# Optimization experiments

Hardware: AMD Instinct MI355X
Metric: run time of the kernel (lower is better)

The kernel has to match this reference:

```python
import jax, jax.numpy as jnp
import numpy as np
from jax import lax

B, T, I, H, O = 1000, 100, 264, 100, 264


def _lstm_cell(x, h, c, Wih, Whh, bih, bhh):
    # PyTorch gate order: i, f, g, o
    gates = x @ Wih.T + bih + h @ Whh.T + bhh  # [B, 4H]
    i, f, g, o = jnp.split(gates, 4, axis=-1)
    i = jax.nn.sigmoid(i)
    f = jax.nn.sigmoid(f)
    g = jnp.tanh(g)
    o = jax.nn.sigmoid(o)
    c = f * c + i * g
    h = o * jnp.tanh(c)
    return h, c


def _encode(src, Wih, Whh, bih, bhh):
    # src: [B, T, I] -> final (h, c), each [B, H]
    x_t = jnp.swapaxes(src, 0, 1)  # [T, B, I]
    h0 = jnp.zeros((src.shape[0], H), src.dtype)
    c0 = jnp.zeros((src.shape[0], H), src.dtype)

    def step(carry, x):
        h, c = carry
        h, c = _lstm_cell(x, h, c, Wih, Whh, bih, bhh)
        return (h, c), None

    (h, c), _ = lax.scan(step, (h0, c0), x_t)
    return h, c


def _decode(h, c, Wih, Whh, bih, bhh, fcW, fcb, batch, steps):
    x0 = jnp.zeros((batch, I), h.dtype)

    def step(carry, _):
        x, hh, cc = carry
        hh, cc = _lstm_cell(x, hh, cc, Wih, Whh, bih, bhh)
        pred = hh @ fcW.T + fcb  # [B, O]
        return (pred, hh, cc), pred

    _, preds = lax.scan(step, (x0, h, c), None, length=steps)
    return jnp.swapaxes(preds, 0, 1)  # [B, T, O]


def setup_inputs():
    key = jax.random.key(0)
    ks = jax.random.split(key, 20)
    bound = 1.0 / np.sqrt(H)

    def u(k, shp):
        return jax.random.uniform(k, shp, jnp.float32, -bound, bound)

    inp = {
        "src": jax.random.normal(ks[0], (B, T, I), jnp.float32),
        "trg": jax.random.normal(ks[1], (B, T, I), jnp.float32),
        "enc_Wih": u(ks[2], (4 * H, I)), "enc_Whh": u(ks[3], (4 * H, H)),
        "enc_bih": u(ks[4], (4 * H,)), "enc_bhh": u(ks[5], (4 * H,)),
        "pd_Wih": u(ks[6], (4 * H, I)), "pd_Whh": u(ks[7], (4 * H, H)),
        "pd_bih": u(ks[8], (4 * H,)), "pd_bhh": u(ks[9], (4 * H,)),
        "pd_fcW": u(ks[10], (O, H)), "pd_fcb": u(ks[11], (O,)),
        "rd_Wih": u(ks[12], (4 * H, I)), "rd_Whh": u(ks[13], (4 * H, H)),
        "rd_bih": u(ks[14], (4 * H,)), "rd_bhh": u(ks[15], (4 * H,)),
        "rd_fcW": u(ks[16], (O, H)), "rd_fcb": u(ks[17], (O,)),
    }
    return inp


def reference(src, trg, enc_Wih, enc_Whh, enc_bih, enc_bhh,
              pd_Wih, pd_Whh, pd_bih, pd_bhh, pd_fcW, pd_fcb,
              rd_Wih, rd_Whh, rd_bih, rd_bhh, rd_fcW, rd_fcb):
    batch, steps, _ = src.shape
    h, c = _encode(src, enc_Wih, enc_Whh, enc_bih, enc_bhh)

    predict_output = _decode(h, c, pd_Wih, pd_Whh, pd_bih, pd_bhh,
                             pd_fcW, pd_fcb, batch, steps)
    predict_loss = jnp.mean((predict_output - trg) ** 2)

    reconstruct_output = _decode(h, c, rd_Wih, rd_Whh, rd_bih, rd_bhh,
                                 rd_fcW, rd_fcb, batch, steps)
    src_rev = src[:, ::-1, :]
    reconstruct_loss = jnp.mean((reconstruct_output - src_rev) ** 2)

    return reconstruct_loss, predict_loss
```

## Files before the change

### kernel.cpp

```cpp
#include <hip/hip_runtime.h>
#include <math.h>

#define NB 1000
#define NT 100
#define NI 264
#define NH 100
#define NO 264
#define NG 400
#define KE 364
#define DM 4
#define NDB 250
#define EDM 4
#define DTH 192
#define XM 16

__device__ __forceinline__ float sigm(float x){ return 1.f / (1.f + __expf(-x)); }
__device__ __forceinline__ float tanh_fast(float x){
    float e = __expf(-2.f * x);
    return 2.f / (1.f + e) - 1.f;
}

#define FMA4(acc, hv, wv) acc += hv.x*wv.x + hv.y*wv.y + hv.z*wv.z + hv.w*wv.w;

#define W_LIST(OP) OP(0) OP(1) OP(2) OP(3) OP(4) OP(5) OP(6) OP(7) OP(8) OP(9) \
                   OP(10) OP(11) OP(12) OP(13) OP(14) OP(15) OP(16) OP(17) OP(18) OP(19) \
                   OP(20) OP(21) OP(22) OP(23) OP(24)

#define DECL_W(i)    float4 w##i = make_float4(0.f, 0.f, 0.f, 0.f);
#define LOADW_ENC(i) w##i = WhhT4[(i) * NG + n];

#define ROW4K(wv, kk) { float4 hq; \
    hq = ((const float4*)sh_h[0])[kk]; FMA4(a0, hq, wv) \
    hq = ((const float4*)sh_h[1])[kk]; FMA4(a1, hq, wv) \
    hq = ((const float4*)sh_h[2])[kk]; FMA4(a2, hq, wv) \
    hq = ((const float4*)sh_h[3])[kk]; FMA4(a3, hq, wv) }

#define ESTEP(i) ROW4K(w##i, i)


__global__ void prep_T4(const float* __restrict__ in, float* __restrict__ out, int N, int K)
{
    int idx = blockIdx.x * 256 + threadIdx.x;
    if (idx >= N * K) return;
    int j  = idx & 3;
    int n  = (idx >> 2) % N;
    int k  = (idx / (4 * N)) * 4 + j;
    out[idx] = in[n * K + k];
}

__global__ void prep_encT(const float* __restrict__ Wih, const float* __restrict__ Whh,
                          float* __restrict__ out)
{
    int idx = blockIdx.x * 256 + threadIdx.x;
    if (idx >= NG * KE) return;
    int j  = idx & 3;
    int n  = (idx >> 2) % NG;
    int k  = (idx / (4 * NG)) * 4 + j;
    out[idx] = (k < NI) ? Wih[n * NI + k] : Whh[n * NH + (k - NI)];
}

__global__ void prep_wdec(const float* __restrict__ Wih, const float* __restrict__ Whh,
                          const float* __restrict__ fcW, float* __restrict__ WdecT)
{
    int idx = blockIdx.x * 256 + threadIdx.x;
    if (idx >= NG * NH) return;
    int n = idx / NH, k = idx - n * NH;
    float acc = Whh[idx];
    const float* wr = Wih + (size_t)n * NI;
    for (int o = 0; o < NI; ++o) acc = fmaf(wr[o], fcW[o * NH + k], acc);
    WdecT[((k >> 2) * NG + n) * 4 + (k & 3)] = acc;
}

__global__ void prep_bias(const float* __restrict__ pb1, const float* __restrict__ pb2,
                          const float* __restrict__ pW,  const float* __restrict__ pfb,
                          const float* __restrict__ rb1, const float* __restrict__ rb2,
                          const float* __restrict__ rW,  const float* __restrict__ rfb,
                          const float* __restrict__ eb1, const float* __restrict__ eb2,
                          float* __restrict__ b0_p, float* __restrict__ bdec_p,
                          float* __restrict__ b0_r, float* __restrict__ bdec_r,
                          float* __restrict__ bcat, float* __restrict__ loss)
{
    int tid = blockIdx.x * 256 + threadIdx.x;
    if (tid < 2) loss[tid] = 0.f;
    if (tid < NG) bcat[tid] = eb1[tid] + eb2[tid];
    if (tid >= 2 * NG) return;
    int dd = tid / NG, n = tid - dd * NG;
    const float* b1 = dd ? rb1 : pb1;
    const float* b2 = dd ? rb2 : pb2;
    const float* W  = dd ? rW  : pW;
    const float* fb = dd ? rfb : pfb;
    float base = b1[n] + b2[n];
    float acc = base;
    const float* wr = W + (size_t)n * NI;
    for (int o = 0; o < NI; ++o) acc = fmaf(wr[o], fb[o], acc);
    if (dd){ b0_r[n] = base; bdec_r[n] = acc; }
    else   { b0_p[n] = base; bdec_p[n] = acc; }
}


__global__ __launch_bounds__(512) void xp_kernel(const float* __restrict__ src,
                                                 const float4* __restrict__ WihT4,
                                                 float* __restrict__ xp)
{
    __shared__ float sh_x[XM * NI];
    __shared__ float sh_o[XM * NG];
    const int tid = threadIdx.x;
    const size_t bt0 = (size_t)blockIdx.x * XM;
    for (int i = tid; i < XM * NI; i += 512) sh_x[i] = src[bt0 * NI + i];
    __syncthreads();
    const bool act = tid < NG;
    const int n = act ? tid : 0;
    float a0=0,a1=0,a2=0,a3=0,a4=0,a5=0,a6=0,a7=0,
          a8=0,a9=0,a10=0,a11=0,a12=0,a13=0,a14=0,a15=0;
    if (act){
        #pragma unroll 3
        for (int k4 = 0; k4 < NI / 4; ++k4){
            float4 wq = WihT4[k4 * NG + n];
            float4 hq;
            #define XROW(r, acc) hq = ((const float4*)(sh_x + (r) * NI))[k4]; FMA4(acc, hq, wq)
            XROW(0,a0)  XROW(1,a1)  XROW(2,a2)  XROW(3,a3)
            XROW(4,a4)  XROW(5,a5)  XROW(6,a6)  XROW(7,a7)
            XROW(8,a8)  XROW(9,a9)  XROW(10,a10) XROW(11,a11)
            XROW(12,a12) XROW(13,a13) XROW(14,a14) XROW(15,a15)
            #undef XROW
        }
        sh_o[0*NG+n]=a0;   sh_o[1*NG+n]=a1;   sh_o[2*NG+n]=a2;   sh_o[3*NG+n]=a3;
        sh_o[4*NG+n]=a4;   sh_o[5*NG+n]=a5;   sh_o[6*NG+n]=a6;   sh_o[7*NG+n]=a7;
        sh_o[8*NG+n]=a8;   sh_o[9*NG+n]=a9;   sh_o[10*NG+n]=a10; sh_o[11*NG+n]=a11;
        sh_o[12*NG+n]=a12; sh_o[13*NG+n]=a13; sh_o[14*NG+n]=a14; sh_o[15*NG+n]=a15;
    }
    __syncthreads();
    for (int i = tid; i < XM * NG; i += 512) xp[bt0 * NG + i] = sh_o[i];
}


__global__ __launch_bounds__(512) __attribute__((amdgpu_waves_per_eu(2, 2)))
void enc_rec(const float* __restrict__ xp,
             const float4* __restrict__ WhhT4,
             const float* __restrict__ bcat,
             float* __restrict__ h_out, float* __restrict__ c_out)
{
    __shared__ float sh_h[EDM][104];
    __shared__ float sh_g[NG][EDM + 1];
    const int tid = threadIdx.x;
    const int b0  = blockIdx.x * EDM;
    const bool act = tid < NG;
    const int n  = act ? tid : 0;
    const int mc = n / NH, jc = n % NH;
    float bias = act ? bcat[n] : 0.f;
    float c0 = 0.f;

    W_LIST(DECL_W)
    if (act){
        W_LIST(LOADW_ENC)
        sh_h[mc][jc] = 0.f;
    }
    __syncthreads();

    for (int t = 0; t < NT; ++t){
        if (act){
            const float* xr = xp + ((size_t)b0 * NT + t) * NG + n;
            float a0 = bias + xr[0 * NT * NG];
            float a1 = bias + xr[1 * NT * NG];
            float a2 = bias + xr[2 * NT * NG];
            float a3 = bias + xr[3 * NT * NG];
            W_LIST(ESTEP)
            sh_g[n][0]=a0; sh_g[n][1]=a1; sh_g[n][2]=a2; sh_g[n][3]=a3;
        }
        __syncthreads();
        if (act){
            float ai = sh_g[jc][mc], af = sh_g[NH + jc][mc];
            float ag = sh_g[2*NH + jc][mc], ao = sh_g[3*NH + jc][mc];
            float ii = sigm(ai), ff = sigm(af), gg = tanh_fast(ag), oo = sigm(ao);
            c0 = ff * c0 + ii * gg;
            sh_h[mc][jc] = oo * tanh_fast(c0);
        }
        __syncthreads();
    }
    if (act){
        h_out[(size_t)(b0 + mc) * NH + jc] = sh_h[mc][jc];
        c_out[(size_t)(b0 + mc) * NH + jc] = c0;
    }
}


__global__ __launch_bounds__(512) void enc_stream(const float* __restrict__ src,
                                                  const float4* __restrict__ WencT4,
                                                  const float* __restrict__ bcat,
                                                  float* __restrict__ h_out, float* __restrict__ c_out)
{
    __shared__ float sh_xh[4][368];
    __shared__ float sh_g[NG][5];
    const int tid = threadIdx.x;
    const int m0  = blockIdx.x * 4;
    const bool act = tid < NG;
    const int n  = act ? tid : 0;
    const int mc = n / NH, jc = n % NH;
    float bias = act ? bcat[n] : 0.f;
    float c_reg = 0.f, h_new = 0.f;
    if (act) sh_xh[mc][NI + jc] = 0.f;
    const float* s0 = src + (size_t)m0 * NT * NI;

    for (int t = 0; t < NT; ++t){
        for (int i = tid; i < 4 * NI; i += 512){
            int r = i / NI, k = i - r * NI;
            sh_xh[r][k] = s0[(size_t)r * NT * NI + (size_t)t * NI + k];
        }
        __syncthreads();
        if (act){
            float a0 = bias, a1 = bias, a2 = bias, a3 = bias;
            #pragma unroll 7
            for (int k4 = 0; k4 < KE / 4; ++k4){
                float4 wq = WencT4[k4 * NG + n];
                float4 hq;
                hq = ((const float4*)sh_xh[0])[k4]; FMA4(a0, hq, wq)
                hq = ((const float4*)sh_xh[1])[k4]; FMA4(a1, hq, wq)
                hq = ((const float4*)sh_xh[2])[k4]; FMA4(a2, hq, wq)
                hq = ((const float4*)sh_xh[3])[k4]; FMA4(a3, hq, wq)
            }
            sh_g[n][0]=a0; sh_g[n][1]=a1; sh_g[n][2]=a2; sh_g[n][3]=a3;
        }
        __syncthreads();
        if (act){
            float ai = sh_g[jc][mc], af = sh_g[NH + jc][mc];
            float ag = sh_g[2*NH + jc][mc], ao = sh_g[3*NH + jc][mc];
            float ii = sigm(ai), ff = sigm(af), gg = tanh_fast(ag), oo = sigm(ao);
            c_reg = ff * c_reg + ii * gg;
            h_new = oo * tanh_fast(c_reg);
            sh_xh[mc][NI + jc] = h_new;
        }
        __syncthreads();
    }
    if (act){
        h_out[(size_t)(m0 + mc) * NH + jc] = h_new;
        c_out[(size_t)(m0 + mc) * NH + jc] = c_reg;
    }
}


__global__ __launch_bounds__(DTH) void decoder_kernel(
    const float* __restrict__ h_enc, const float* __restrict__ c_enc,
    const float4* __restrict__ WhhT_p, const float4* __restrict__ WdecT_p,
    const float* __restrict__ b0_p,  const float* __restrict__ bdec_p,
    const float4* __restrict__ fcWT_p, const float* __restrict__ fcb_p,
    const float* __restrict__ trg,
    const float4* __restrict__ WhhT_r, const float4* __restrict__ WdecT_r,
    const float* __restrict__ b0_r,  const float* __restrict__ bdec_r,
    const float4* __restrict__ fcWT_r, const float* __restrict__ fcb_r,
    const float* __restrict__ src,
    float* __restrict__ loss)
{
    __shared__ float sh_h[DM][104];
    __shared__ float sh_g[NG][DM + 1];
    __shared__ float sh_red[3];
    const int tid = threadIdx.x;
    const int d   = (blockIdx.x >= NDB) ? 1 : 0;
    const int m0  = (blockIdx.x - d * NDB) * DM;
    const float4* WhhT  = d ? WhhT_r  : WhhT_p;
    const float4* WdecT = d ? WdecT_r : WdecT_p;
    const float*  b0    = d ? b0_r    : b0_p;
    const float*  bdec  = d ? bdec_r  : bdec_p;
    const float4* fcWT  = d ? fcWT_r  : fcWT_p;
    const float*  fcb   = d ? fcb_r   : fcb_p;
    const float*  tgt   = d ? src     : trg;

    const bool gate = tid < NH;
    const bool fc   = (tid >= 128) && (tid < 192);
    const int n  = gate ? tid : 0;
    const int o  = fc ? tid - 128 : 0;
    const bool fcx = fc && (o < 8);

    float bz0=0,bz1=0,bz2=0,bz3=0, bd0=0,bd1=0,bd2=0,bd3=0;
    float fb0=0,fb1=0,fb2=0,fb3=0,fb4=0;
    if (gate){
        bz0=b0[n];        bz1=b0[n+NH];     bz2=b0[n+2*NH];   bz3=b0[n+3*NH];
        bd0=bdec[n];      bd1=bdec[n+NH];   bd2=bdec[n+2*NH]; bd3=bdec[n+3*NH];
    } else if (fc){
        fb0=fcb[o]; fb1=fcb[o+64]; fb2=fcb[o+128]; fb3=fcb[o+192];
        if (fcx) fb4=fcb[o+256];
    }

    float c0=0.f, c1=0.f, c2=0.f, c3=0.f;
    if (gate){
        c0 = c_enc[(size_t)(m0+0)*NH + n];
        c1 = c_enc[(size_t)(m0+1)*NH + n];
        c2 = c_enc[(size_t)(m0+2)*NH + n];
        c3 = c_enc[(size_t)(m0+3)*NH + n];
        sh_h[0][n] = h_enc[(size_t)(m0+0)*NH + n];
        sh_h[1][n] = h_enc[(size_t)(m0+1)*NH + n];
        sh_h[2][n] = h_enc[(size_t)(m0+2)*NH + n];
        sh_h[3][n] = h_enc[(size_t)(m0+3)*NH + n];
    }
    float loss_acc = 0.f;
    __syncthreads();

    for (int k = 0; k <= NT; ++k){
        if (gate && k < NT){
            const float4* WT = (k == 0) ? WhhT : WdecT;
            float biasA = k ? bd0 : bz0, biasB = k ? bd1 : bz1;
            float biasC = k ? bd2 : bz2, biasD = k ? bd3 : bz3;
            float A0=biasA,A1=biasA,A2=biasA,A3=biasA;
            float B0=biasB,B1=biasB,B2=biasB,B3=biasB;
            float C0=biasC,C1=biasC,C2=biasC,C3=biasC;
            float D0=biasD,D1=biasD,D2=biasD,D3=biasD;
            #pragma unroll 5
            for (int k4 = 0; k4 < NH / 4; ++k4){
                float4 wa = WT[k4 * NG + n];
                float4 wb = WT[k4 * NG + n + NH];
                float4 wc = WT[k4 * NG + n + 2*NH];
                float4 wd = WT[k4 * NG + n + 3*NH];
                float4 h0q = ((const float4*)sh_h[0])[k4];
                float4 h1q = ((const float4*)sh_h[1])[k4];
                float4 h2q = ((const float4*)sh_h[2])[k4];
                float4 h3q = ((const float4*)sh_h[3])[k4];
                FMA4(A0,h0q,wa) FMA4(A1,h1q,wa) FMA4(A2,h2q,wa) FMA4(A3,h3q,wa)
                FMA4(B0,h0q,wb) FMA4(B1,h1q,wb) FMA4(B2,h2q,wb) FMA4(B3,h3q,wb)
                FMA4(C0,h0q,wc) FMA4(C1,h1q,wc) FMA4(C2,h2q,wc) FMA4(C3,h3q,wc)
                FMA4(D0,h0q,wd) FMA4(D1,h1q,wd) FMA4(D2,h2q,wd) FMA4(D3,h3q,wd)
            }
            sh_g[n][0]=A0;        sh_g[n][1]=A1;        sh_g[n][2]=A2;        sh_g[n][3]=A3;
            sh_g[n+NH][0]=B0;     sh_g[n+NH][1]=B1;     sh_g[n+NH][2]=B2;     sh_g[n+NH][3]=B3;
            sh_g[n+2*NH][0]=C0;   sh_g[n+2*NH][1]=C1;   sh_g[n+2*NH][2]=C2;   sh_g[n+2*NH][3]=C3;
            sh_g[n+3*NH][0]=D0;   sh_g[n+3*NH][1]=D1;   sh_g[n+3*NH][2]=D2;   sh_g[n+3*NH][3]=D3;
        } else if (fc && k >= 1){
            float P0=fb0,P1=fb0,P2=fb0,P3=fb0;
            float Q0=fb1,Q1=fb1,Q2=fb1,Q3=fb1;
            float R0=fb2,R1=fb2,R2=fb2,R3=fb2;
            float S0=fb3,S1=fb3,S2=fb3,S3=fb3;
            float T0=fb4,T1=fb4,T2=fb4,T3=fb4;
            #pragma unroll 5
            for (int k4 = 0; k4 < NH / 4; ++k4){
                float4 wa = fcWT[k4 * NO + o];
                float4 wb = fcWT[k4 * NO + o + 64];
                float4 wc = fcWT[k4 * NO + o + 128];
                float4 wd = fcWT[k4 * NO + o + 192];
                float4 h0q = ((const float4*)sh_h[0])[k4];
                float4 h1q = ((const float4*)sh_h[1])[k4];
                float4 h2q = ((const float4*)sh_h[2])[k4];
                float4 h3q = ((const float4*)sh_h[3])[k4];
                FMA4(P0,h0q,wa) FMA4(P1,h1q,wa) FMA4(P2,h2q,wa) FMA4(P3,h3q,wa)
                FMA4(Q0,h0q,wb) FMA4(Q1,h1q,wb) FMA4(Q2,h2q,wb) FMA4(Q3,h3q,wb)
                FMA4(R0,h0q,wc) FMA4(R1,h1q,wc) FMA4(R2,h2q,wc) FMA4(R3,h3q,wc)
                FMA4(S0,h0q,wd) FMA4(S1,h1q,wd) FMA4(S2,h2q,wd) FMA4(S3,h3q,wd)
                if (fcx){
                    float4 we = fcWT[k4 * NO + o + 256];
                    FMA4(T0,h0q,we) FMA4(T1,h1q,we) FMA4(T2,h2q,we) FMA4(T3,h3q,we)
                }
            }
            const int ti = d ? (NT - k) : (k - 1);
            const float* tg = tgt + (size_t)m0 * NT * NI + (size_t)ti * NI;
            float df;
            df = P0 - tg[0*NT*NI + o];       loss_acc += df * df;
            df = P1 - tg[1*NT*NI + o];       loss_acc += df * df;
            df = P2 - tg[2*NT*NI + o];       loss_acc += df * df;
            df = P3 - tg[3*NT*NI + o];       loss_acc += df * df;
            df = Q0 - tg[0*NT*NI + o + 64];  loss_acc += df * df;
            df = Q1 - tg[1*NT*NI + o + 64];  loss_acc += df * df;
            df = Q2 - tg[2*NT*NI + o + 64];  loss_acc += df * df;
            df = Q3 - tg[3*NT*NI + o + 64];  loss_acc += df * df;
            df = R0 - tg[0*NT*NI + o + 128]; loss_acc += df * df;
            df = R1 - tg[1*NT*NI + o + 128]; loss_acc += df * df;
            df = R2 - tg[2*NT*NI + o + 128]; loss_acc += df * df;
            df = R3 - tg[3*NT*NI + o + 128]; loss_acc += df * df;
            df = S0 - tg[0*NT*NI + o + 192]; loss_acc += df * df;
            df = S1 - tg[1*NT*NI + o + 192]; loss_acc += df * df;
            df = S2 - tg[2*NT*NI + o + 192]; loss_acc += df * df;
            df = S3 - tg[3*NT*NI + o + 192]; loss_acc += df * df;
            if (fcx){
                df = T0 - tg[0*NT*NI + o + 256]; loss_acc += df * df;
                df = T1 - tg[1*NT*NI + o + 256]; loss_acc += df * df;
                df = T2 - tg[2*NT*NI + o + 256]; loss_acc += df * df;
                df = T3 - tg[3*NT*NI + o + 256]; loss_acc += df * df;
            }
        }
        __syncthreads();
        if (gate && k < NT){
            #define ACT(r, cc) { \
                float ai = sh_g[n][r], af = sh_g[NH + n][r]; \
                float ag = sh_g[2*NH + n][r], ao = sh_g[3*NH + n][r]; \
                float ii = sigm(ai), ff = sigm(af), gg = tanh_fast(ag), oo = sigm(ao); \
                cc = ff * cc + ii * gg; \
                sh_h[r][n] = oo * tanh_fast(cc); }
            ACT(0, c0) ACT(1, c1) ACT(2, c2) ACT(3, c3)
            #undef ACT
        }
        __syncthreads();
    }

    for (int off = 32; off > 0; off >>= 1) loss_acc += __shfl_down(loss_acc, off);
    if ((tid & 63) == 0) sh_red[tid >> 6] = loss_acc;
    __syncthreads();
    if (tid == 0){
        float s = sh_red[0] + sh_red[1] + sh_red[2];
        atomicAdd(&loss[d], s);
    }
}

__global__ void finalize_kernel(const float* __restrict__ loss, float* __restrict__ out){
    if (threadIdx.x == 0){
        const float inv = 1.f / 26400000.f;
        out[0] = loss[1] * inv;
        out[1] = loss[0] * inv;
    }
}

extern "C" void kernel_launch(void* const* d_in, const int* in_sizes, int n_in,
                              void* d_out, int out_size, void* d_ws, size_t ws_size,
                              hipStream_t stream)
{
    const float* src  = (const float*)d_in[0];
    const float* trg  = (const float*)d_in[1];
    const float* eWih = (const float*)d_in[2];
    const float* eWhh = (const float*)d_in[3];
    const float* ebih = (const float*)d_in[4];
    const float* ebhh = (const float*)d_in[5];
    const float* pWih = (const float*)d_in[6];
    const float* pWhh = (const float*)d_in[7];
    const float* pbih = (const float*)d_in[8];
    const float* pbhh = (const float*)d_in[9];
    const float* pfcW = (const float*)d_in[10];
    const float* pfcb = (const float*)d_in[11];
    const float* rWih = (const float*)d_in[12];
    const float* rWhh = (const float*)d_in[13];
    const float* rbih = (const float*)d_in[14];
    const float* rbhh = (const float*)d_in[15];
    const float* rfcW = (const float*)d_in[16];
    const float* rfcb = (const float*)d_in[17];

    float* w       = (float*)d_ws;
    float* WihT4e  = w;
    float* WencT4  = w + 105600;
    float* WhhT4e  = w + 251200;
    float* WdT_p   = w + 291200;
    float* WdT_r   = w + 331200;
    float* WhT_p   = w + 371200;
    float* WhT_r   = w + 411200;
    float* fcT_p   = w + 451200;
    float* fcT_r   = w + 477600;
    float* b0_p    = w + 504000;
    float* bdec_p  = w + 504400;
    float* b0_r    = w + 504800;
    float* bdec_r  = w + 505200;
    float* bcat    = w + 505600;
    float* h_enc   = w + 506000;
    float* c_enc   = w + 606000;
    float* loss    = w + 706000;
    float* XP      = w + 706016;
    const bool big = ws_size >= (size_t)(706016 + 40000000) * 4;

    const int TB = 256;
    if (big){
        prep_T4<<<(NG*NI + TB-1)/TB, TB, 0, stream>>>(eWih, WihT4e, NG, NI);
        prep_T4<<<(NG*NH + TB-1)/TB, TB, 0, stream>>>(eWhh, WhhT4e, NG, NH);
    } else {
        prep_encT<<<(NG*KE + TB-1)/TB, TB, 0, stream>>>(eWih, eWhh, WencT4);
    }
    prep_T4<<<(NG*NH + TB-1)/TB, TB, 0, stream>>>(pWhh, WhT_p, NG, NH);
    prep_T4<<<(NG*NH + TB-1)/TB, TB, 0, stream>>>(rWhh, WhT_r, NG, NH);
    prep_T4<<<(NO*NH + TB-1)/TB, TB, 0, stream>>>(pfcW, fcT_p, NO, NH);
    prep_T4<<<(NO*NH + TB-1)/TB, TB, 0, stream>>>(rfcW, fcT_r, NO, NH);
    prep_wdec<<<(NG*NH + TB-1)/TB, TB, 0, stream>>>(pWih, pWhh, pfcW, WdT_p);
    prep_wdec<<<(NG*NH + TB-1)/TB, TB, 0, stream>>>(rWih, rWhh, rfcW, WdT_r);
    prep_bias<<<4, TB, 0, stream>>>(pbih, pbhh, pWih, pfcb, rbih, rbhh, rWih, rfcb,
                                    ebih, ebhh, b0_p, bdec_p, b0_r, bdec_r, bcat, loss);

    if (big){
        xp_kernel<<<(NB*NT)/XM, 512, 0, stream>>>(src, (const float4*)WihT4e, XP);
        enc_rec<<<NB/EDM, 512, 0, stream>>>(XP, (const float4*)WhhT4e, bcat, h_enc, c_enc);
    } else {
        enc_stream<<<NB/4, 512, 0, stream>>>(src, (const float4*)WencT4, bcat, h_enc, c_enc);
    }
    decoder_kernel<<<2 * NDB, DTH, 0, stream>>>(h_enc, c_enc,
        (const float4*)WhT_p, (const float4*)WdT_p, b0_p, bdec_p, (const float4*)fcT_p, pfcb, trg,
        (const float4*)WhT_r, (const float4*)WdT_r, b0_r, bdec_r, (const float4*)fcT_r, rfcb, src,
        loss);
    finalize_kernel<<<1, 64, 0, stream>>>(loss, (float*)d_out);
}
```

Baseline: 2.290 ms.

## Split decoder gate and FC dot products across two K-halves with LDS reduction

Doubles the decoder block to 384 threads and splits the hidden-dimension reduction of both the gate matmul and the FC projection into two K-halves, each handled by its own group of threads. Partial sums go into doubled shared buffers and are added during the activation and loss phases, which halves the serial dependent FMA chain per step of the recurrence. In exchange it uses more shared memory and adds extra shared-memory traffic for the partial sums. Larger blocks may also reduce how many blocks fit on each CU.

Result: faster. 2.236 ms (-2.3%).

```diff
diff --git a/kernel.cpp b/kernel.cpp
--- a/kernel.cpp
+++ b/kernel.cpp
@@ -11,7 +11,7 @@
 #define DM 4
 #define NDB 250
 #define EDM 4
-#define DTH 192
+#define DTH 384
 #define XM 16
 
 __device__ __forceinline__ float sigm(float x){ return 1.f / (1.f + __expf(-x)); }
@@ -251,8 +251,9 @@
     float* __restrict__ loss)
 {
     __shared__ float sh_h[DM][104];
-    __shared__ float sh_g[NG][DM + 1];
-    __shared__ float sh_red[3];
+    __shared__ float sh_g[2][NG][DM + 1];
+    __shared__ float sh_fp[2][64][21];
+    __shared__ float sh_red[6];
     const int tid = threadIdx.x;
     const int d   = (blockIdx.x >= NDB) ? 1 : 0;
     const int m0  = (blockIdx.x - d * NDB) * DM;
@@ -264,24 +265,31 @@
     const float*  fcb   = d ? fcb_r   : fcb_p;
     const float*  tgt   = d ? src     : trg;
 
-    const bool gate = tid < NH;
-    const bool fc   = (tid >= 128) && (tid < 192);
-    const int n  = gate ? tid : 0;
-    const int o  = fc ? tid - 128 : 0;
+    const bool gate0 = tid < NH;
+    const bool gate1 = (tid >= 128) && (tid < 128 + NH);
+    const bool gate  = gate0 || gate1;
+    const bool fc0   = (tid >= 256) && (tid < 320);
+    const bool fc1   = (tid >= 320);
+    const bool fc    = fc0 || fc1;
+    const int n  = gate1 ? (tid - 128) : tid;
+    const int o  = fc1 ? (tid - 320) : (tid - 256);
     const bool fcx = fc && (o < 8);
+    const int kg   = (gate1 || fc1) ? 1 : 0;
+    const int KS   = kg ? 13 : 0;
+    const int KEND = kg ? 25 : 13;
 
     float bz0=0,bz1=0,bz2=0,bz3=0, bd0=0,bd1=0,bd2=0,bd3=0;
     float fb0=0,fb1=0,fb2=0,fb3=0,fb4=0;
-    if (gate){
-        bz0=b0[n];        bz1=b0[n+NH];     bz2=b0[n+2*NH];   bz3=b0[n+3*NH];
-        bd0=bdec[n];      bd1=bdec[n+NH];   bd2=bdec[n+2*NH]; bd3=bdec[n+3*NH];
-    } else if (fc){
+    if (gate0){
+        bz0=b0[n];   bz1=b0[n+NH];   bz2=b0[n+2*NH];   bz3=b0[n+3*NH];
+        bd0=bdec[n]; bd1=bdec[n+NH]; bd2=bdec[n+2*NH]; bd3=bdec[n+3*NH];
+    } else if (fc0){
         fb0=fcb[o]; fb1=fcb[o+64]; fb2=fcb[o+128]; fb3=fcb[o+192];
         if (fcx) fb4=fcb[o+256];
     }
 
     float c0=0.f, c1=0.f, c2=0.f, c3=0.f;
-    if (gate){
+    if (gate0){
         c0 = c_enc[(size_t)(m0+0)*NH + n];
         c1 = c_enc[(size_t)(m0+1)*NH + n];
         c2 = c_enc[(size_t)(m0+2)*NH + n];
@@ -297,14 +305,20 @@
     for (int k = 0; k <= NT; ++k){
         if (gate && k < NT){
             const float4* WT = (k == 0) ? WhhT : WdecT;
-            float biasA = k ? bd0 : bz0, biasB = k ? bd1 : bz1;
-            float biasC = k ? bd2 : bz2, biasD = k ? bd3 : bz3;
-            float A0=biasA,A1=biasA,A2=biasA,A3=biasA;
-            float B0=biasB,B1=biasB,B2=biasB,B3=biasB;
-            float C0=biasC,C1=biasC,C2=biasC,C3=biasC;
-            float D0=biasD,D1=biasD,D2=biasD,D3=biasD;
-            #pragma unroll 5
-            for (int k4 = 0; k4 < NH / 4; ++k4){
+            float A0,A1,A2,A3,B0,B1,B2,B3,C0,C1,C2,C3,D0,D1,D2,D3;
+            if (kg == 0){
+                float biasA = k ? bd0 : bz0, biasB = k ? bd1 : bz1;
+                float biasC = k ? bd2 : bz2, biasD = k ? bd3 : bz3;
+                A0=biasA;A1=biasA;A2=biasA;A3=biasA;
+                B0=biasB;B1=biasB;B2=biasB;B3=biasB;
+                C0=biasC;C1=biasC;C2=biasC;C3=biasC;
+                D0=biasD;D1=biasD;D2=biasD;D3=biasD;
+            } else {
+                A0=0;A1=0;A2=0;A3=0; B0=0;B1=0;B2=0;B3=0;
+                C0=0;C1=0;C2=0;C3=0; D0=0;D1=0;D2=0;D3=0;
+            }
+            #pragma unroll 4
+            for (int k4 = KS; k4 < KEND; ++k4){
                 float4 wa = WT[k4 * NG + n];
                 float4 wb = WT[k4 * NG + n + NH];
                 float4 wc = WT[k4 * NG + n + 2*NH];
@@ -318,18 +332,23 @@
                 FMA4(C0,h0q,wc) FMA4(C1,h1q,wc) FMA4(C2,h2q,wc) FMA4(C3,h3q,wc)
                 FMA4(D0,h0q,wd) FMA4(D1,h1q,wd) FMA4(D2,h2q,wd) FMA4(D3,h3q,wd)
             }
-            sh_g[n][0]=A0;        sh_g[n][1]=A1;        sh_g[n][2]=A2;        sh_g[n][3]=A3;
-            sh_g[n+NH][0]=B0;     sh_g[n+NH][1]=B1;     sh_g[n+NH][2]=B2;     sh_g[n+NH][3]=B3;
-            sh_g[n+2*NH][0]=C0;   sh_g[n+2*NH][1]=C1;   sh_g[n+2*NH][2]=C2;   sh_g[n+2*NH][3]=C3;
-            sh_g[n+3*NH][0]=D0;   sh_g[n+3*NH][1]=D1;   sh_g[n+3*NH][2]=D2;   sh_g[n+3*NH][3]=D3;
+            sh_g[kg][n][0]=A0;        sh_g[kg][n][1]=A1;        sh_g[kg][n][2]=A2;        sh_g[kg][n][3]=A3;
+            sh_g[kg][n+NH][0]=B0;     sh_g[kg][n+NH][1]=B1;     sh_g[kg][n+NH][2]=B2;     sh_g[kg][n+NH][3]=B3;
+            sh_g[kg][n+2*NH][0]=C0;   sh_g[kg][n+2*NH][1]=C1;   sh_g[kg][n+2*NH][2]=C2;   sh_g[kg][n+2*NH][3]=C3;
+            sh_g[kg][n+3*NH][0]=D0;   sh_g[kg][n+3*NH][1]=D1;   sh_g[kg][n+3*NH][2]=D2;   sh_g[kg][n+3*NH][3]=D3;
         } else if (fc && k >= 1){
-            float P0=fb0,P1=fb0,P2=fb0,P3=fb0;
-            float Q0=fb1,Q1=fb1,Q2=fb1,Q3=fb1;
-            float R0=fb2,R1=fb2,R2=fb2,R3=fb2;
-            float S0=fb3,S1=fb3,S2=fb3,S3=fb3;
-            float T0=fb4,T1=fb4,T2=fb4,T3=fb4;
-            #pragma unroll 5
-            for (int k4 = 0; k4 < NH / 4; ++k4){
+            float P0,P1,P2,P3,Q0,Q1,Q2,Q3,R0,R1,R2,R3,S0,S1,S2,S3,T0,T1,T2,T3;
+            if (kg == 0){
+                P0=fb0;P1=fb0;P2=fb0;P3=fb0; Q0=fb1;Q1=fb1;Q2=fb1;Q3=fb1;
+                R0=fb2;R1=fb2;R2=fb2;R3=fb2; S0=fb3;S1=fb3;S2=fb3;S3=fb3;
+                T0=fb4;T1=fb4;T2=fb4;T3=fb4;
+            } else {
+                P0=0;P1=0;P2=0;P3=0; Q0=0;Q1=0;Q2=0;Q3=0;
+                R0=0;R1=0;R2=0;R3=0; S0=0;S1=0;S2=0;S3=0;
+                T0=0;T1=0;T2=0;T3=0;
+            }
+            #pragma unroll 4
+            for (int k4 = KS; k4 < KEND; ++k4){
                 float4 wa = fcWT[k4 * NO + o];
                 float4 wb = fcWT[k4 * NO + o + 64];
                 float4 wc = fcWT[k4 * NO + o + 128];
@@ -347,42 +366,38 @@
                     FMA4(T0,h0q,we) FMA4(T1,h1q,we) FMA4(T2,h2q,we) FMA4(T3,h3q,we)
                 }
             }
-            const int ti = d ? (NT - k) : (k - 1);
-            const float* tg = tgt + (size_t)m0 * NT * NI + (size_t)ti * NI;
-            float df;
-            df = P0 - tg[0*NT*NI + o];       loss_acc += df * df;
-            df = P1 - tg[1*NT*NI + o];       loss_acc += df * df;
-            df = P2 - tg[2*NT*NI + o];       loss_acc += df * df;
-            df = P3 - tg[3*NT*NI + o];       loss_acc += df * df;
-            df = Q0 - tg[0*NT*NI + o + 64];  loss_acc += df * df;
-            df = Q1 - tg[1*NT*NI + o + 64];  loss_acc += df * df;
-            df = Q2 - tg[2*NT*NI + o + 64];  loss_acc += df * df;
-            df = Q3 - tg[3*NT*NI + o + 64];  loss_acc += df * df;
-            df = R0 - tg[0*NT*NI + o + 128]; loss_acc += df * df;
-            df = R1 - tg[1*NT*NI + o + 128]; loss_acc += df * df;
-            df = R2 - tg[2*NT*NI + o + 128]; loss_acc += df * df;
-            df = R3 - tg[3*NT*NI + o + 128]; loss_acc += df * df;
-            df = S0 - tg[0*NT*NI + o + 192]; loss_acc += df * df;
-            df = S1 - tg[1*NT*NI + o + 192]; loss_acc += df * df;
-            df = S2 - tg[2*NT*NI + o + 192]; loss_acc += df * df;
-            df = S3 - tg[3*NT*NI + o + 192]; loss_acc += df * df;
-            if (fcx){
-                df = T0 - tg[0*NT*NI + o + 256]; loss_acc += df * df;
-                df = T1 - tg[1*NT*NI + o + 256]; loss_acc += df * df;
-                df = T2 - tg[2*NT*NI + o + 256]; loss_acc += df * df;
-                df = T3 - tg[3*NT*NI + o + 256]; loss_acc += df * df;
-            }
-        }
-        __syncthreads();
-        if (gate && k < NT){
+            float (*fp)[21] = sh_fp[kg];
+            fp[o][0]=P0;  fp[o][1]=P1;  fp[o][2]=P2;  fp[o][3]=P3;
+            fp[o][4]=Q0;  fp[o][5]=Q1;  fp[o][6]=Q2;  fp[o][7]=Q3;
+            fp[o][8]=R0;  fp[o][9]=R1;  fp[o][10]=R2; fp[o][11]=R3;
+            fp[o][12]=S0; fp[o][13]=S1; fp[o][14]=S2; fp[o][15]=S3;
+            if (fcx){ fp[o][16]=T0; fp[o][17]=T1; fp[o][18]=T2; fp[o][19]=T3; }
+        }
+        __syncthreads();
+        if (gate0 && k < NT){
             #define ACT(r, cc) { \
-                float ai = sh_g[n][r], af = sh_g[NH + n][r]; \
-                float ag = sh_g[2*NH + n][r], ao = sh_g[3*NH + n][r]; \
+                float ai = sh_g[0][n][r]      + sh_g[1][n][r]; \
+                float af = sh_g[0][NH+n][r]   + sh_g[1][NH+n][r]; \
+                float ag = sh_g[0][2*NH+n][r] + sh_g[1][2*NH+n][r]; \
+                float ao = sh_g[0][3*NH+n][r] + sh_g[1][3*NH+n][r]; \
                 float ii = sigm(ai), ff = sigm(af), gg = tanh_fast(ag), oo = sigm(ao); \
                 cc = ff * cc + ii * gg; \
                 sh_h[r][n] = oo * tanh_fast(cc); }
             ACT(0, c0) ACT(1, c1) ACT(2, c2) ACT(3, c3)
             #undef ACT
+        } else if (fc && k >= 1){
+            const int ti = d ? (NT - k) : (k - 1);
+            const float* tg = tgt + (size_t)m0 * NT * NI + (size_t)ti * NI;
+            const int r0 = 2*kg, r1 = 2*kg + 1;
+            float s, df;
+            #define LOSSCOL(ci, coff) \
+                s = sh_fp[0][o][(ci)*4+r0] + sh_fp[1][o][(ci)*4+r0]; \
+                df = s - tg[(size_t)r0*NT*NI + (coff)]; loss_acc += df*df; \
+                s = sh_fp[0][o][(ci)*4+r1] + sh_fp[1][o][(ci)*4+r1]; \
+                df = s - tg[(size_t)r1*NT*NI + (coff)]; loss_acc += df*df;
+            LOSSCOL(0, o) LOSSCOL(1, o+64) LOSSCOL(2, o+128) LOSSCOL(3, o+192)
+            if (fcx){ LOSSCOL(4, o+256) }
+            #undef LOSSCOL
         }
         __syncthreads();
     }
@@ -391,7 +406,8 @@
     if ((tid & 63) == 0) sh_red[tid >> 6] = loss_acc;
     __syncthreads();
     if (tid == 0){
-        float s = sh_red[0] + sh_red[1] + sh_red[2];
+        float s = 0.f;
+        for (int w = 0; w < 6; ++w) s += sh_red[w];
         atomicAdd(&loss[d], s);
     }
 }
```

## Double-buffer decoder hidden state and process eight batch rows per block

Applied to the files above, without the earlier changes.

The decoder block now handles eight batch rows instead of four, which halves the block count and doubles reuse of each weight load from global memory. Each gate thread applies the LSTM activations directly from its registers and writes the new hidden state into a ping-pong shared buffer. This removes the shared gate staging array and one of the two barriers per timestep. The trade-off is roughly double the accumulator registers per thread, which may lower occupancy or cause spills, and only 250 blocks are launched.

Result: slower. 2.727 ms (+19.1%).

```diff
diff --git a/kernel.cpp b/kernel.cpp
--- a/kernel.cpp
+++ b/kernel.cpp
@@ -8,8 +8,8 @@
 #define NO 264
 #define NG 400
 #define KE 364
-#define DM 4
-#define NDB 250
+#define DM 8
+#define NDB 125
 #define EDM 4
 #define DTH 192
 #define XM 16
@@ -250,8 +250,7 @@
     const float* __restrict__ src,
     float* __restrict__ loss)
 {
-    __shared__ float sh_h[DM][104];
-    __shared__ float sh_g[NG][DM + 1];
+    __shared__ float sh_h[2][DM][104];
     __shared__ float sh_red[3];
     const int tid = threadIdx.x;
     const int d   = (blockIdx.x >= NDB) ? 1 : 0;
@@ -273,118 +272,131 @@
     float bz0=0,bz1=0,bz2=0,bz3=0, bd0=0,bd1=0,bd2=0,bd3=0;
     float fb0=0,fb1=0,fb2=0,fb3=0,fb4=0;
     if (gate){
-        bz0=b0[n];        bz1=b0[n+NH];     bz2=b0[n+2*NH];   bz3=b0[n+3*NH];
-        bd0=bdec[n];      bd1=bdec[n+NH];   bd2=bdec[n+2*NH]; bd3=bdec[n+3*NH];
+        bz0=b0[n];   bz1=b0[n+NH];   bz2=b0[n+2*NH];   bz3=b0[n+3*NH];
+        bd0=bdec[n]; bd1=bdec[n+NH]; bd2=bdec[n+2*NH]; bd3=bdec[n+3*NH];
     } else if (fc){
         fb0=fcb[o]; fb1=fcb[o+64]; fb2=fcb[o+128]; fb3=fcb[o+192];
         if (fcx) fb4=fcb[o+256];
     }
 
-    float c0=0.f, c1=0.f, c2=0.f, c3=0.f;
+    float cc0=0,cc1=0,cc2=0,cc3=0,cc4=0,cc5=0,cc6=0,cc7=0;
     if (gate){
-        c0 = c_enc[(size_t)(m0+0)*NH + n];
-        c1 = c_enc[(size_t)(m0+1)*NH + n];
-        c2 = c_enc[(size_t)(m0+2)*NH + n];
-        c3 = c_enc[(size_t)(m0+3)*NH + n];
-        sh_h[0][n] = h_enc[(size_t)(m0+0)*NH + n];
-        sh_h[1][n] = h_enc[(size_t)(m0+1)*NH + n];
-        sh_h[2][n] = h_enc[(size_t)(m0+2)*NH + n];
-        sh_h[3][n] = h_enc[(size_t)(m0+3)*NH + n];
+        cc0 = c_enc[(size_t)(m0+0)*NH + n];
+        cc1 = c_enc[(size_t)(m0+1)*NH + n];
+        cc2 = c_enc[(size_t)(m0+2)*NH + n];
+        cc3 = c_enc[(size_t)(m0+3)*NH + n];
+        cc4 = c_enc[(size_t)(m0+4)*NH + n];
+        cc5 = c_enc[(size_t)(m0+5)*NH + n];
+        cc6 = c_enc[(size_t)(m0+6)*NH + n];
+        cc7 = c_enc[(size_t)(m0+7)*NH + n];
+        sh_h[0][0][n] = h_enc[(size_t)(m0+0)*NH + n];
+        sh_h[0][1][n] = h_enc[(size_t)(m0+1)*NH + n];
+        sh_h[0][2][n] = h_enc[(size_t)(m0+2)*NH + n];
+        sh_h[0][3][n] = h_enc[(size_t)(m0+3)*NH + n];
+        sh_h[0][4][n] = h_enc[(size_t)(m0+4)*NH + n];
+        sh_h[0][5][n] = h_enc[(size_t)(m0+5)*NH + n];
+        sh_h[0][6][n] = h_enc[(size_t)(m0+6)*NH + n];
+        sh_h[0][7][n] = h_enc[(size_t)(m0+7)*NH + n];
     }
     float loss_acc = 0.f;
     __syncthreads();
 
+    int p = 0;
     for (int k = 0; k <= NT; ++k){
         if (gate && k < NT){
             const float4* WT = (k == 0) ? WhhT : WdecT;
             float biasA = k ? bd0 : bz0, biasB = k ? bd1 : bz1;
             float biasC = k ? bd2 : bz2, biasD = k ? bd3 : bz3;
-            float A0=biasA,A1=biasA,A2=biasA,A3=biasA;
-            float B0=biasB,B1=biasB,B2=biasB,B3=biasB;
-            float C0=biasC,C1=biasC,C2=biasC,C3=biasC;
-            float D0=biasD,D1=biasD,D2=biasD,D3=biasD;
+            float A0=biasA,A1=biasA,A2=biasA,A3=biasA,A4=biasA,A5=biasA,A6=biasA,A7=biasA;
+            float B0=biasB,B1=biasB,B2=biasB,B3=biasB,B4=biasB,B5=biasB,B6=biasB,B7=biasB;
+            float C0=biasC,C1=biasC,C2=biasC,C3=biasC,C4=biasC,C5=biasC,C6=biasC,C7=biasC;
+            float D0=biasD,D1=biasD,D2=biasD,D3=biasD,D4=biasD,D5=biasD,D6=biasD,D7=biasD;
+            const float (*hb)[104] = sh_h[p];
             #pragma unroll 5
             for (int k4 = 0; k4 < NH / 4; ++k4){
                 float4 wa = WT[k4 * NG + n];
                 float4 wb = WT[k4 * NG + n + NH];
                 float4 wc = WT[k4 * NG + n + 2*NH];
                 float4 wd = WT[k4 * NG + n + 3*NH];
-                float4 h0q = ((const float4*)sh_h[0])[k4];
-                float4 h1q = ((const float4*)sh_h[1])[k4];
-                float4 h2q = ((const float4*)sh_h[2])[k4];
-                float4 h3q = ((const float4*)sh_h[3])[k4];
+                float4 h0q = ((const float4*)hb[0])[k4];
+                float4 h1q = ((const float4*)hb[1])[k4];
+                float4 h2q = ((const float4*)hb[2])[k4];
+                float4 h3q = ((const float4*)hb[3])[k4];
+                float4 h4q = ((const float4*)hb[4])[k4];
+                float4 h5q = ((const float4*)hb[5])[k4];
+                float4 h6q = ((const float4*)hb[6])[k4];
+                float4 h7q = ((const float4*)hb[7])[k4];
                 FMA4(A0,h0q,wa) FMA4(A1,h1q,wa) FMA4(A2,h2q,wa) FMA4(A3,h3q,wa)
+                FMA4(A4,h4q,wa) FMA4(A5,h5q,wa) FMA4(A6,h6q,wa) FMA4(A7,h7q,wa)
                 FMA4(B0,h0q,wb) FMA4(B1,h1q,wb) FMA4(B2,h2q,wb) FMA4(B3,h3q,wb)
+                FMA4(B4,h4q,wb) FMA4(B5,h5q,wb) FMA4(B6,h6q,wb) FMA4(B7,h7q,wb)
                 FMA4(C0,h0q,wc) FMA4(C1,h1q,wc) FMA4(C2,h2q,wc) FMA4(C3,h3q,wc)
+                FMA4(C4,h4q,wc) FMA4(C5,h5q,wc) FMA4(C6,h6q,wc) FMA4(C7,h7q,wc)
                 FMA4(D0,h0q,wd) FMA4(D1,h1q,wd) FMA4(D2,h2q,wd) FMA4(D3,h3q,wd)
+                FMA4(D4,h4q,wd) FMA4(D5,h5q,wd) FMA4(D6,h6q,wd) FMA4(D7,h7q,wd)
             }
-            sh_g[n][0]=A0;        sh_g[n][1]=A1;        sh_g[n][2]=A2;        sh_g[n][3]=A3;
-            sh_g[n+NH][0]=B0;     sh_g[n+NH][1]=B1;     sh_g[n+NH][2]=B2;     sh_g[n+NH][3]=B3;
-            sh_g[n+2*NH][0]=C0;   sh_g[n+2*NH][1]=C1;   sh_g[n+2*NH][2]=C2;   sh_g[n+2*NH][3]=C3;
-            sh_g[n+3*NH][0]=D0;   sh_g[n+3*NH][1]=D1;   sh_g[n+3*NH][2]=D2;   sh_g[n+3*NH][3]=D3;
+            float (*hn)[104] = sh_h[p ^ 1];
+            #define ACT(r, Ar, Br, Cr, Dr, cc) { \
+                float ii = sigm(Ar), ff = sigm(Br), gg = tanh_fast(Cr), oo = sigm(Dr); \
+                cc = ff * cc + ii * gg; \
+                hn[r][n] = oo * tanh_fast(cc); }
+            ACT(0,A0,B0,C0,D0,cc0) ACT(1,A1,B1,C1,D1,cc1)
+            ACT(2,A2,B2,C2,D2,cc2) ACT(3,A3,B3,C3,D3,cc3)
+            ACT(4,A4,B4,C4,D4,cc4) ACT(5,A5,B5,C5,D5,cc5)
+            ACT(6,A6,B6,C6,D6,cc6) ACT(7,A7,B7,C7,D7,cc7)
+            #undef ACT
         } else if (fc && k >= 1){
-            float P0=fb0,P1=fb0,P2=fb0,P3=fb0;
-            float Q0=fb1,Q1=fb1,Q2=fb1,Q3=fb1;
-            float R0=fb2,R1=fb2,R2=fb2,R3=fb2;
-            float S0=fb3,S1=fb3,S2=fb3,S3=fb3;
-            float T0=fb4,T1=fb4,T2=fb4,T3=fb4;
+            float P0=fb0,P1=fb0,P2=fb0,P3=fb0,P4=fb0,P5=fb0,P6=fb0,P7=fb0;
+            float Q0=fb1,Q1=fb1,Q2=fb1,Q3=fb1,Q4=fb1,Q5=fb1,Q6=fb1,Q7=fb1;
+            float R0=fb2,R1=fb2,R2=fb2,R3=fb2,R4=fb2,R5=fb2,R6=fb2,R7=fb2;
+            float S0=fb3,S1=fb3,S2=fb3,S3=fb3,S4=fb3,S5=fb3,S6=fb3,S7=fb3;
+            float T0=fb4,T1=fb4,T2=fb4,T3=fb4,T4=fb4,T5=fb4,T6=fb4,T7=fb4;
+            const float (*hb)[104] = sh_h[p];
             #pragma unroll 5
             for (int k4 = 0; k4 < NH / 4; ++k4){
                 float4 wa = fcWT[k4 * NO + o];
                 float4 wb = fcWT[k4 * NO + o + 64];
                 float4 wc = fcWT[k4 * NO + o + 128];
                 float4 wd = fcWT[k4 * NO + o + 192];
-                float4 h0q = ((const float4*)sh_h[0])[k4];
-                float4 h1q = ((const float4*)sh_h[1])[k4];
-                float4 h2q = ((const float4*)sh_h[2])[k4];
-                float4 h3q = ((const float4*)sh_h[3])[k4];
+                float4 h0q = ((const float4*)hb[0])[k4];
+                float4 h1q = ((const float4*)hb[1])[k4];
+                float4 h2q = ((const float4*)hb[2])[k4];
+                float4 h3q = ((const float4*)hb[3])[k4];
+                float4 h4q = ((const float4*)hb[4])[k4];
+                float4 h5q = ((const float4*)hb[5])[k4];
+                float4 h6q = ((const float4*)hb[6])[k4];
+                float4 h7q = ((const float4*)hb[7])[k4];
                 FMA4(P0,h0q,wa) FMA4(P1,h1q,wa) FMA4(P2,h2q,wa) FMA4(P3,h3q,wa)
+                FMA4(P4,h4q,wa) FMA4(P5,h5q,wa) FMA4(P6,h6q,wa) FMA4(P7,h7q,wa)
                 FMA4(Q0,h0q,wb) FMA4(Q1,h1q,wb) FMA4(Q2,h2q,wb) FMA4(Q3,h3q,wb)
+                FMA4(Q4,h4q,wb) FMA4(Q5,h5q,wb) FMA4(Q6,h6q,wb) FMA4(Q7,h7q,wb)
                 FMA4(R0,h0q,wc) FMA4(R1,h1q,wc) FMA4(R2,h2q,wc) FMA4(R3,h3q,wc)
+                FMA4(R4,h4q,wc) FMA4(R5,h5q,wc) FMA4(R6,h6q,wc) FMA4(R7,h7q,wc)
                 FMA4(S0,h0q,wd) FMA4(S1,h1q,wd) FMA4(S2,h2q,wd) FMA4(S3,h3q,wd)
+                FMA4(S4,h4q,wd) FMA4(S5,h5q,wd) FMA4(S6,h6q,wd) FMA4(S7,h7q,wd)
                 if (fcx){
                     float4 we = fcWT[k4 * NO + o + 256];
                     FMA4(T0,h0q,we) FMA4(T1,h1q,we) FMA4(T2,h2q,we) FMA4(T3,h3q,we)
+                    FMA4(T4,h4q,we) FMA4(T5,h5q,we) FMA4(T6,h6q,we) FMA4(T7,h7q,we)
                 }
             }
             const int ti = d ? (NT - k) : (k - 1);
             const float* tg = tgt + (size_t)m0 * NT * NI + (size_t)ti * NI;
             float df;
-            df = P0 - tg[0*NT*NI + o];       loss_acc += df * df;
-            df = P1 - tg[1*NT*NI + o];       loss_acc += df * df;
-            df = P2 - tg[2*NT*NI + o];       loss_acc += df * df;
-            df = P3 - tg[3*NT*NI + o];       loss_acc += df * df;
-            df = Q0 - tg[0*NT*NI + o + 64];  loss_acc += df * df;
-            df = Q1 - tg[1*NT*NI + o + 64];  loss_acc += df * df;
-            df = Q2 - tg[2*NT*NI + o + 64];  loss_acc += df * df;
-            df = Q3 - tg[3*NT*NI + o + 64];  loss_acc += df * df;
-            df = R0 - tg[0*NT*NI + o + 128]; loss_acc += df * df;
-            df = R1 - tg[1*NT*NI + o + 128]; loss_acc += df * df;
-            df = R2 - tg[2*NT*NI + o + 128]; loss_acc += df * df;
-            df = R3 - tg[3*NT*NI + o + 128]; loss_acc += df * df;
-            df = S0 - tg[0*NT*NI + o + 192]; loss_acc += df * df;
-            df = S1 - tg[1*NT*NI + o + 192]; loss_acc += df * df;
-            df = S2 - tg[2*NT*NI + o + 192]; loss_acc += df * df;
-            df = S3 - tg[3*NT*NI + o + 192]; loss_acc += df * df;
-            if (fcx){
-                df = T0 - tg[0*NT*NI + o + 256]; loss_acc += df * df;
-                df = T1 - tg[1*NT*NI + o + 256]; loss_acc += df * df;
-                df = T2 - tg[2*NT*NI + o + 256]; loss_acc += df * df;
-                df = T3 - tg[3*NT*NI + o + 256]; loss_acc += df * df;
-            }
-        }
-        __syncthreads();
-        if (gate && k < NT){
-            #define ACT(r, cc) { \
-                float ai = sh_g[n][r], af = sh_g[NH + n][r]; \
-                float ag = sh_g[2*NH + n][r], ao = sh_g[3*NH + n][r]; \
-                float ii = sigm(ai), ff = sigm(af), gg = tanh_fast(ag), oo = sigm(ao); \
-                cc = ff * cc + ii * gg; \
-                sh_h[r][n] = oo * tanh_fast(cc); }
-            ACT(0, c0) ACT(1, c1) ACT(2, c2) ACT(3, c3)
-            #undef ACT
-        }
-        __syncthreads();
+            #define LROW(r, Pr, Qr, Rr, Sr, Tr) \
+                df = Pr - tg[(size_t)(r)*NT*NI + o];       loss_acc += df*df; \
+                df = Qr - tg[(size_t)(r)*NT*NI + o + 64];  loss_acc += df*df; \
+                df = Rr - tg[(size_t)(r)*NT*NI + o + 128]; loss_acc += df*df; \
+                df = Sr - tg[(size_t)(r)*NT*NI + o + 192]; loss_acc += df*df; \
+                if (fcx){ df = Tr - tg[(size_t)(r)*NT*NI + o + 256]; loss_acc += df*df; }
+            LROW(0,P0,Q0,R0,S0,T0) LROW(1,P1,Q1,R1,S1,T1)
+            LROW(2,P2,Q2,R2,S2,T2) LROW(3,P3,Q3,R3,S3,T3)
+            LROW(4,P4,Q4,R4,S4,T4) LROW(5,P5,Q5,R5,S5,T5)
+            LROW(6,P6,Q6,R6,S6,T6) LROW(7,P7,Q7,R7,S7,T7)
+            #undef LROW
+        }
+        __syncthreads();
+        p ^= 1;
     }
 
     for (int off = 32; off > 0; off >>= 1) loss_acc += __shfl_down(loss_acc, off);
```
